# Kernel tuning notes

Measured on AMD Instinct MI355X. Metric: run time of the kernel, lower is better.

Reference implementation:

```python
import jax, jax.numpy as jnp
import numpy as np

B, D_IN, D_Z, N_TRIALS = 4096, 784, 128, 256
T_TEMP = 1.0  # PVAE.t


def setup_inputs() -> dict:
    key = jax.random.key(0)
    ks = jax.random.split(key, 4)
    x = jax.random.normal(ks[0], (B, D_IN), jnp.float32)
    # uniform base samples for reparameterized Exponential(rate) draws
    u = jax.random.uniform(ks[1], (N_TRIALS, B, D_Z), jnp.float32,
                           minval=1e-7, maxval=1.0 - 1e-7)
    W_enc = jax.random.normal(ks[2], (D_IN, D_Z), jnp.float32) * 0.03
    b_enc = jnp.zeros((D_Z,), jnp.float32)
    W_dec = jax.random.normal(ks[3], (D_Z, D_IN), jnp.float32) * 0.08
    b_dec = jnp.zeros((D_IN,), jnp.float32)
    prior = jnp.zeros((1, D_Z), jnp.float32)
    return {"x": x, "u": u, "W_enc": W_enc, "b_enc": b_enc,
            "W_dec": W_dec, "b_dec": b_dec, "prior": prior}


def reference(x, u, W_enc, b_enc, W_dec, b_dec, prior):
    # encoder: du = clamp(Linear(x), max=5)
    du = jnp.minimum(x @ W_enc + b_enc, 5.0)                 # [B, Z]
    # log_rate = clamp(du + clamp(prior, max=5), max=5); rate = exp(.) + 1e-6
    log_rate = jnp.minimum(du + jnp.minimum(prior, 5.0), 5.0)
    rate = jnp.exp(log_rate) + 1e-6                          # [B, Z]
    # exponential race: e ~ Exp(1) via inverse CDF, scaled by 1/rate
    e = -jnp.log1p(-u)                                       # [T, B, Z]
    times = jnp.cumsum(e / rate[None], axis=0)               # prefix sums of arrival times
    # soft indicator (training path, t = 1.0): sigmoid((1 - times) / t)
    indicator = jax.nn.sigmoid((1.0 - times) / T_TEMP)       # [T, B, Z]
    z = jnp.sum(indicator, axis=0)                           # [B, Z] soft Poisson count
    # decoder: sigmoid(Linear(z))
    y = jax.nn.sigmoid(z @ W_dec + b_dec)                    # [B, 784]
    return (du, z, y)
```

## Files before the change

kernel.cpp:

```cpp
#include <hip/hip_runtime.h>
#include <cstdint>
#include <cstddef>

#define LOG2E 1.44269504088896340736f
#define LN2   0.69314718055994530942f

__device__ __forceinline__ float fast_log2(float x) { return __builtin_amdgcn_logf(x); }
__device__ __forceinline__ float fast_exp2(float x) { return __builtin_amdgcn_exp2f(x); }
__device__ __forceinline__ float fast_rcp(float x)  { return __builtin_amdgcn_rcpf(x); }


__global__ __launch_bounds__(256) void enc_kernel(const float* __restrict__ x,
                                                  const float* __restrict__ W,
                                                  const float* __restrict__ bias,
                                                  float* __restrict__ du) {
  __shared__ float xs[16][16];
  __shared__ float ws[16][128];
  const int tid  = threadIdx.x;
  const int row0 = blockIdx.x * 16;
  const int cg   = tid & 31;
  const int rg   = tid >> 5;

  float4 a0 = {0.f, 0.f, 0.f, 0.f};
  float4 a1 = {0.f, 0.f, 0.f, 0.f};

  for (int k0 = 0; k0 < 784; k0 += 16) {
    __syncthreads();
    if (tid < 64) {
      int r = tid >> 2, kc = (tid & 3) * 4;
      *(float4*)&xs[r][kc] = *(const float4*)&x[(size_t)(row0 + r) * 784 + k0 + kc];
    }
#pragma unroll
    for (int j = 0; j < 2; j++) {
      int i = tid + 256 * j;
      int k = i >> 5, c4 = (i & 31) * 4;
      *(float4*)&ws[k][c4] = *(const float4*)&W[(size_t)(k0 + k) * 128 + c4];
    }
    __syncthreads();
#pragma unroll
    for (int k = 0; k < 16; k++) {
      float x0 = xs[rg * 2][k];
      float x1 = xs[rg * 2 + 1][k];
      float4 w = *(const float4*)&ws[k][cg * 4];
      a0.x = fmaf(x0, w.x, a0.x); a0.y = fmaf(x0, w.y, a0.y);
      a0.z = fmaf(x0, w.z, a0.z); a0.w = fmaf(x0, w.w, a0.w);
      a1.x = fmaf(x1, w.x, a1.x); a1.y = fmaf(x1, w.y, a1.y);
      a1.z = fmaf(x1, w.z, a1.z); a1.w = fmaf(x1, w.w, a1.w);
    }
  }

  float4 bb = *(const float4*)&bias[cg * 4];
  float4 r0, r1;
  r0.x = fminf(a0.x + bb.x, 5.f); r0.y = fminf(a0.y + bb.y, 5.f);
  r0.z = fminf(a0.z + bb.z, 5.f); r0.w = fminf(a0.w + bb.w, 5.f);
  r1.x = fminf(a1.x + bb.x, 5.f); r1.y = fminf(a1.y + bb.y, 5.f);
  r1.z = fminf(a1.z + bb.z, 5.f); r1.w = fminf(a1.w + bb.w, 5.f);
  *(float4*)&du[(size_t)(row0 + rg * 2)     * 128 + cg * 4] = r0;
  *(float4*)&du[(size_t)(row0 + rg * 2 + 1) * 128 + cg * 4] = r1;
}

__global__ __launch_bounds__(256) void race_kernel(const float* __restrict__ u,
                                                   const float* __restrict__ du,
                                                   const float* __restrict__ prior,
                                                   float* __restrict__ zout) {
  const int g  = blockIdx.x * 256 + threadIdx.x;
  const int b  = g >> 5;
  const int z4 = (g & 31) * 4;

  const float4 d = *(const float4*)&du[(size_t)b * 128 + z4];
  const float4 p = *(const float4*)&prior[z4];

  float sinv[4];
  {
    const float dd[4] = {d.x, d.y, d.z, d.w};
    const float pp[4] = {p.x, p.y, p.z, p.w};
#pragma unroll
    for (int j = 0; j < 4; j++) {
      float lr   = fminf(dd[j] + fminf(pp[j], 5.f), 5.f);
      float rate = fast_exp2(lr * LOG2E) + 1e-6f;
      sinv[j]    = -LN2 / rate;
    }
  }

  float t[4]   = {0.f, 0.f, 0.f, 0.f};
  float acc[4] = {0.f, 0.f, 0.f, 0.f};
  const float* up = u + (size_t)b * 128 + z4;
  const float TMAX = 18.f;

  for (int tt = 0; tt < 256; tt += 2) {
    bool act = fminf(fminf(t[0], t[1]), fminf(t[2], t[3])) < TMAX;
    if (!__any(act)) break;
    if (act) {
      float4 ua = *(const float4*)&up[(size_t)tt * (4096 * 128)];
      float4 ub = *(const float4*)&up[(size_t)(tt + 1) * (4096 * 128)];
      const float uaj[4] = {ua.x, ua.y, ua.z, ua.w};
      const float ubj[4] = {ub.x, ub.y, ub.z, ub.w};
#pragma unroll
      for (int j = 0; j < 4; j++) {
        float l = fast_log2(1.f - uaj[j]);
        t[j] = fmaf(l, sinv[j], t[j]);
        float e = fast_exp2(fmaf(t[j], LOG2E, -LOG2E));
        acc[j] += fast_rcp(1.f + e);
        l = fast_log2(1.f - ubj[j]);
        t[j] = fmaf(l, sinv[j], t[j]);
        e = fast_exp2(fmaf(t[j], LOG2E, -LOG2E));
        acc[j] += fast_rcp(1.f + e);
      }
    }
  }

  float4 r; r.x = acc[0]; r.y = acc[1]; r.z = acc[2]; r.w = acc[3];
  *(float4*)&zout[(size_t)b * 128 + z4] = r;
}

__global__ __launch_bounds__(256) void dec_kernel(const float* __restrict__ z,
                                                  const float* __restrict__ W,
                                                  const float* __restrict__ bias,
                                                  float* __restrict__ y) {
  __shared__ float zs[8 * 128];
  const int tid = threadIdx.x;
  const int b0  = blockIdx.x * 8;
  *(float4*)&zs[tid * 4] = *(const float4*)&z[(size_t)b0 * 128 + tid * 4];
  __syncthreads();

  for (int col = tid; col < 784; col += 256) {
    float bv = bias[col];
    float acc[8];
#pragma unroll
    for (int i = 0; i < 8; i++) acc[i] = bv;
#pragma unroll 4
    for (int k = 0; k < 128; k++) {
      float w = W[(size_t)k * 784 + col];
#pragma unroll
      for (int i = 0; i < 8; i++) acc[i] = fmaf(zs[i * 128 + k], w, acc[i]);
    }
#pragma unroll
    for (int i = 0; i < 8; i++) {
      float ex = fast_exp2(-acc[i] * LOG2E);
      y[(size_t)(b0 + i) * 784 + col] = fast_rcp(1.f + ex);
    }
  }
}

extern "C" void kernel_launch(void* const* d_in, const int* in_sizes, int n_in,
                              void* d_out, int out_size, void* d_ws, size_t ws_size,
                              hipStream_t stream) {
  const float* x     = (const float*)d_in[0];
  const float* u     = (const float*)d_in[1];
  const float* W_enc = (const float*)d_in[2];
  const float* b_enc = (const float*)d_in[3];
  const float* W_dec = (const float*)d_in[4];
  const float* b_dec = (const float*)d_in[5];
  const float* prior = (const float*)d_in[6];

  float* out = (float*)d_out;
  float* du  = out;
  float* zz  = out + 4096 * 128;
  float* y   = out + 2 * 4096 * 128;

  enc_kernel <<<256, 256, 0, stream>>>(x, W_enc, b_enc, du);
  race_kernel<<<512, 256, 0, stream>>>(u, du, prior, zz);
  dec_kernel <<<512, 256, 0, stream>>>(zz, W_dec, b_dec, y);
}
```

Baseline: 788.1 us.

## Prefetch race samples, halve per-thread work, and register-tile decoder columns

The race kernel now handles two latent dims per thread with twice as many blocks, and software-prefetches the next pair of uniform samples before computing the current step, moving the early-exit check to the loop end. The decoder drops the shared-memory staging of z and instead has each thread accumulate all four of its output columns at once, reading z as float4 directly from global memory. The intent is to hide memory latency on the sample stream, sharpen per-wave early exit, and reuse z loads across columns. The cost is an extra speculative load at the final iteration, narrower float2 loads, and more registers in the decoder.

```diff
diff --git a/kernel.cpp b/kernel.cpp
--- a/kernel.cpp
+++ b/kernel.cpp
@@ -64,81 +64,112 @@
                                                    const float* __restrict__ prior,
                                                    float* __restrict__ zout) {
   const int g  = blockIdx.x * 256 + threadIdx.x;
-  const int b  = g >> 5;
-  const int z4 = (g & 31) * 4;
+  const int b  = g >> 6;
+  const int z2 = (g & 63) * 2;
 
-  const float4 d = *(const float4*)&du[(size_t)b * 128 + z4];
-  const float4 p = *(const float4*)&prior[z4];
+  const float2 d = *(const float2*)&du[(size_t)b * 128 + z2];
+  const float2 p = *(const float2*)&prior[z2];
 
-  float sinv[4];
+  float sinv[2];
   {
-    const float dd[4] = {d.x, d.y, d.z, d.w};
-    const float pp[4] = {p.x, p.y, p.z, p.w};
+    const float dd[2] = {d.x, d.y};
+    const float pp[2] = {p.x, p.y};
 #pragma unroll
-    for (int j = 0; j < 4; j++) {
+    for (int j = 0; j < 2; j++) {
       float lr   = fminf(dd[j] + fminf(pp[j], 5.f), 5.f);
       float rate = fast_exp2(lr * LOG2E) + 1e-6f;
       sinv[j]    = -LN2 / rate;
     }
   }
 
-  float t[4]   = {0.f, 0.f, 0.f, 0.f};
-  float acc[4] = {0.f, 0.f, 0.f, 0.f};
-  const float* up = u + (size_t)b * 128 + z4;
+  float t[2]   = {0.f, 0.f};
+  float acc[2] = {0.f, 0.f};
+  const float* up = u + (size_t)b * 128 + z2;
   const float TMAX = 18.f;
+  const size_t STRIDE = (size_t)4096 * 128;
+
+  float2 c0 = *(const float2*)&up[0];
+  float2 c1 = *(const float2*)&up[STRIDE];
 
   for (int tt = 0; tt < 256; tt += 2) {
-    bool act = fminf(fminf(t[0], t[1]), fminf(t[2], t[3])) < TMAX;
-    if (!__any(act)) break;
+    bool act = fminf(t[0], t[1]) < TMAX;
+    float2 n0, n1;
+    {
+      int tn = (tt + 2 < 256) ? (tt + 2) : 254;
+      if (act) {
+        n0 = *(const float2*)&up[(size_t)tn * STRIDE];
+        n1 = *(const float2*)&up[(size_t)(tn + 1) * STRIDE];
+      }
+    }
     if (act) {
-      float4 ua = *(const float4*)&up[(size_t)tt * (4096 * 128)];
-      float4 ub = *(const float4*)&up[(size_t)(tt + 1) * (4096 * 128)];
-      const float uaj[4] = {ua.x, ua.y, ua.z, ua.w};
-      const float ubj[4] = {ub.x, ub.y, ub.z, ub.w};
+      const float ua[2] = {c0.x, c0.y};
+      const float ub[2] = {c1.x, c1.y};
 #pragma unroll
-      for (int j = 0; j < 4; j++) {
-        float l = fast_log2(1.f - uaj[j]);
+      for (int j = 0; j < 2; j++) {
+        float l = fast_log2(1.f - ua[j]);
         t[j] = fmaf(l, sinv[j], t[j]);
         float e = fast_exp2(fmaf(t[j], LOG2E, -LOG2E));
         acc[j] += fast_rcp(1.f + e);
-        l = fast_log2(1.f - ubj[j]);
+        l = fast_log2(1.f - ub[j]);
         t[j] = fmaf(l, sinv[j], t[j]);
         e = fast_exp2(fmaf(t[j], LOG2E, -LOG2E));
         acc[j] += fast_rcp(1.f + e);
       }
     }
+    c0 = n0; c1 = n1;
+    if (!__any(fminf(t[0], t[1]) < TMAX)) break;
   }
 
-  float4 r; r.x = acc[0]; r.y = acc[1]; r.z = acc[2]; r.w = acc[3];
-  *(float4*)&zout[(size_t)b * 128 + z4] = r;
+  float2 r; r.x = acc[0]; r.y = acc[1];
+  *(float2*)&zout[(size_t)b * 128 + z2] = r;
 }
 
 __global__ __launch_bounds__(256) void dec_kernel(const float* __restrict__ z,
                                                   const float* __restrict__ W,
                                                   const float* __restrict__ bias,
                                                   float* __restrict__ y) {
-  __shared__ float zs[8 * 128];
   const int tid = threadIdx.x;
   const int b0  = blockIdx.x * 8;
-  *(float4*)&zs[tid * 4] = *(const float4*)&z[(size_t)b0 * 128 + tid * 4];
-  __syncthreads();
+  const float* zb = z + (size_t)b0 * 128;
 
-  for (int col = tid; col < 784; col += 256) {
-    float bv = bias[col];
-    float acc[8];
+  const int c0 = tid, c1 = tid + 256, c2 = tid + 512, c3 = tid + 768;
+  const bool v3 = (c3 < 784);
+
+  float acc0[8], acc1[8], acc2[8], acc3[8];
+  {
+    float bv0 = bias[c0], bv1 = bias[c1], bv2 = bias[c2];
+    float bv3 = v3 ? bias[c3] : 0.f;
 #pragma unroll
-    for (int i = 0; i < 8; i++) acc[i] = bv;
-#pragma unroll 4
-    for (int k = 0; k < 128; k++) {
-      float w = W[(size_t)k * 784 + col];
+    for (int i = 0; i < 8; i++) { acc0[i] = bv0; acc1[i] = bv1; acc2[i] = bv2; acc3[i] = bv3; }
+  }
+
+  for (int k0 = 0; k0 < 128; k0 += 4) {
+    float4 zq[8];
 #pragma unroll
-      for (int i = 0; i < 8; i++) acc[i] = fmaf(zs[i * 128 + k], w, acc[i]);
+    for (int i = 0; i < 8; i++) zq[i] = *(const float4*)&zb[i * 128 + k0];
+#pragma unroll
+    for (int j = 0; j < 4; j++) {
+      const float* Wr = &W[(size_t)(k0 + j) * 784];
+      float w0 = Wr[c0], w1 = Wr[c1], w2 = Wr[c2];
+      float w3 = v3 ? Wr[c3] : 0.f;
+#pragma unroll
+      for (int i = 0; i < 8; i++) {
+        float zv = (j == 0) ? zq[i].x : (j == 1) ? zq[i].y : (j == 2) ? zq[i].z : zq[i].w;
+        acc0[i] = fmaf(zv, w0, acc0[i]);
+        acc1[i] = fmaf(zv, w1, acc1[i]);
+        acc2[i] = fmaf(zv, w2, acc2[i]);
+        acc3[i] = fmaf(zv, w3, acc3[i]);
+      }
     }
+  }
+
 #pragma unroll
-    for (int i = 0; i < 8; i++) {
-      float ex = fast_exp2(-acc[i] * LOG2E);
-      y[(size_t)(b0 + i) * 784 + col] = fast_rcp(1.f + ex);
-    }
+  for (int i = 0; i < 8; i++) {
+    size_t row = (size_t)(b0 + i) * 784;
+    y[row + c0] = fast_rcp(1.f + fast_exp2(-acc0[i] * LOG2E));
+    y[row + c1] = fast_rcp(1.f + fast_exp2(-acc1[i] * LOG2E));
+    y[row + c2] = fast_rcp(1.f + fast_exp2(-acc2[i] * LOG2E));
+    if (v3) y[row + c3] = fast_rcp(1.f + fast_exp2(-acc3[i] * LOG2E));
   }
 }
 
@@ -158,7 +189,7 @@
   float* zz  = out + 4096 * 128;
   float* y   = out + 2 * 4096 * 128;
 
-  enc_kernel <<<256, 256, 0, stream>>>(x, W_enc, b_enc, du);
-  race_kernel<<<512, 256, 0, stream>>>(u, du, prior, zz);
-  dec_kernel <<<512, 256, 0, stream>>>(zz, W_dec, b_dec, y);
+  enc_kernel <<<256,  256, 0, stream>>>(x, W_enc, b_enc, du);
+  race_kernel<<<1024, 256, 0, stream>>>(u, du, prior, zz);
+  dec_kernel <<<512,  256, 0, stream>>>(zz, W_dec, b_dec, y);
 }
```

After: 859.3 us. 9.0% more time.
